# Performance work log

Hardware: AMD Instinct MI355X
Metric: run time of the kernel (lower is better)

## Reference

```python
import jax, jax.numpy as jnp
import numpy as np

B, C, R = 8, 256, 14
H_HEADS = 4
KD = 16            # key_dim
D_V = 64           # attn_ratio * key_dim
KS = 5             # dw conv kernel
N = R * R * R      # tokens


def _bias_idx():
    # replicate original offset logic: only first two coords (|dx|,|dy|) used
    pts = np.array(np.meshgrid(np.arange(R), np.arange(R), np.arange(R), indexing='ij'))
    pts = pts.reshape(3, -1).T  # (N, 3) in itertools.product order
    dx = np.abs(pts[:, 0:1] - pts[None, :, 0])  # (N, N)
    dy = np.abs(pts[:, 1:2] - pts[None, :, 1])
    return (dx * R + dy).astype(np.int32)  # (N, N), values in [0, R*R)


def setup_inputs() -> dict:
    key = jax.random.key(0)
    ks = jax.random.split(key, 12)
    cph = C // H_HEADS
    qkv_out = 2 * KD + D_V
    inp = {
        'x': jax.random.normal(ks[0], (B, C, R, R, R), jnp.float32),
        'Wqkv': jax.random.normal(ks[1], (H_HEADS, qkv_out, cph), jnp.float32) * 0.05,
        'qkv_scale': 1.0 + 0.05 * jax.random.normal(ks[2], (H_HEADS, qkv_out), jnp.float32),
        'qkv_bias': 0.05 * jax.random.normal(ks[3], (H_HEADS, qkv_out), jnp.float32),
        'Wdw': jax.random.normal(ks[4], (H_HEADS, KD, 1, KS, KS, KS), jnp.float32) * 0.05,
        'dw_scale': 1.0 + 0.05 * jax.random.normal(ks[5], (H_HEADS, KD), jnp.float32),
        'dw_bias': 0.05 * jax.random.normal(ks[6], (H_HEADS, KD), jnp.float32),
        'Wproj': jax.random.normal(ks[7], (C, D_V * H_HEADS), jnp.float32) * 0.02,
        'proj_scale': 1.0 + 0.05 * jax.random.normal(ks[8], (C,), jnp.float32),
        'proj_bias': 0.05 * jax.random.normal(ks[9], (C,), jnp.float32),
        'attention_biases': 0.02 * jax.random.normal(ks[10], (H_HEADS, R * R), jnp.float32),
        'bias_idx': jnp.asarray(_bias_idx()),
    }
    return inp


def reference(x, Wqkv, qkv_scale, qkv_bias, Wdw, dw_scale, dw_bias,
              Wproj, proj_scale, proj_bias, attention_biases, bias_idx):
    scale = KD ** (-0.5)
    ab = attention_biases[:, bias_idx]  # (h, N, N) relative-position bias gather
    feats_in = jnp.split(x, H_HEADS, axis=1)  # h x (B, C/h, R, R, R)
    dn = ('NCDHW', 'OIDHW', 'NCDHW')
    feats_out = []
    feat = feats_in[0]
    for i in range(H_HEADS):
        if i > 0:
            feat = feat + feats_in[i]
        # 1x1x1 conv QKV + fused BN (inference-style scale/shift)
        y = jnp.einsum('oc,bcxyz->boxyz', Wqkv[i], feat)
        y = y * qkv_scale[i][:, None, None, None] + qkv_bias[i][:, None, None, None]
        q = y[:, :KD]
        k = y[:, KD:2 * KD]
        v = y[:, 2 * KD:]
        # depthwise conv on q + fused BN
        q = jax.lax.conv_general_dilated(q, Wdw[i], (1, 1, 1), 'SAME',
                                         feature_group_count=KD, dimension_numbers=dn)
        q = q * dw_scale[i][:, None, None, None] + dw_bias[i][:, None, None, None]
        qf = q.reshape(B, KD, N)
        kf = k.reshape(B, KD, N)
        vf = v.reshape(B, D_V, N)
        attn = jnp.einsum('bcn,bcm->bnm', qf, kf) * scale + ab[i]  # (B, N, N)
        attn = jax.nn.softmax(attn, axis=-1)
        feat = jnp.einsum('bcm,bnm->bcn', vf, attn).reshape(B, D_V, R, R, R)
        feats_out.append(feat)
    h = jax.nn.relu(jnp.concatenate(feats_out, axis=1))  # (B, d*h, R, R, R)
    out = jnp.einsum('oc,bcxyz->boxyz', Wproj, h)
    out = out * proj_scale[:, None, None, None] + proj_bias[:, None, None, None]
    return out
```

## Files before the change

kernel.cpp:

```cpp
#include <hip/hip_runtime.h>

#define B_    8
#define C_    256
#define R_    14
#define R2    196
#define N3    2744
#define NP    2752
#define NH    4
#define KD    16
#define DV    64
#define QKVO  96
#define MT    64
#define NTILE 43
#define SPLIT 4
#define TPC   11

#define SC2   0.36067376f
#define LOG2E 1.44269504f

typedef __attribute__((ext_vector_type(8))) short short8v;
typedef __attribute__((ext_vector_type(4))) short short4v;
typedef __attribute__((ext_vector_type(4))) float float4v;

__device__ __forceinline__ int iabs(int v){ return v < 0 ? -v : v; }

__device__ __forceinline__ short f2bf(float f){
    union { float f; unsigned int u; } c; c.f = f;
    return (short)((c.u + 0x7FFFu + ((c.u >> 16) & 1u)) >> 16);
}
__device__ __forceinline__ float bf2f(short s){
    union { unsigned int u; float f; } c; c.u = ((unsigned int)(unsigned short)s) << 16;
    return c.f;
}

__global__ __launch_bounds__(256)
void wprep_kernel(const float* __restrict__ Wp, short* __restrict__ whi,
                  short* __restrict__ wlo, const float* __restrict__ Wqkv,
                  const float* __restrict__ qsc, short* __restrict__ wqhi,
                  short* __restrict__ wqlo)
{
    int i = blockIdx.x * 256 + threadIdx.x;
    {
        float w = Wp[i];
        short hi = f2bf(w);
        short lo = f2bf(w - bf2f(hi));
        whi[i] = hi; wlo[i] = lo;
    }
    if (i < NH * QKVO * 64) {
        int o_all = i >> 6;
        float w = Wqkv[i] * qsc[o_all];
        short hi = f2bf(w);
        short lo = f2bf(w - bf2f(hi));
        wqhi[i] = hi; wqlo[i] = lo;
    }
}

__global__ __launch_bounds__(256, 2)
void qkv_mfma(const float* __restrict__ x, const float* __restrict__ h,
              const short* __restrict__ wqhi, const short* __restrict__ wqlo,
              const float* __restrict__ qbi,
              float* __restrict__ q0, short* __restrict__ kbf, short* __restrict__ vbf,
              int head)
{
    __shared__ short fhi[64][72];
    __shared__ short flo[64][72];
    __shared__ float bsh[96];

    const int b = blockIdx.y;
    const int n0 = blockIdx.x * 64;
    const int t = threadIdx.x;
    const int w = t >> 6, l = t & 63, g = l >> 4, ln = l & 15;

    if (t < 96) bsh[t] = qbi[head * QKVO + t];

    {
        const int sc_ = t & 63;
        const int sng = (t >> 6) * 16;
        const float* xs = x + ((size_t)b * C_ + head * DV + sc_) * N3 + n0 + sng;
        const float* hs = h + ((size_t)b * C_ + (head - 1) * DV + sc_) * N3 + n0 + sng;
        float fv[16];
        if (n0 + sng + 15 < N3) {
#pragma unroll
            for (int e4 = 0; e4 < 4; e4++) {
                float4 xv = ((const float4*)xs)[e4];
                fv[4*e4+0] = xv.x; fv[4*e4+1] = xv.y; fv[4*e4+2] = xv.z; fv[4*e4+3] = xv.w;
            }
            if (head > 0) {
#pragma unroll
                for (int e4 = 0; e4 < 4; e4++) {
                    float4 hv = ((const float4*)hs)[e4];
                    fv[4*e4+0] += hv.x; fv[4*e4+1] += hv.y; fv[4*e4+2] += hv.z; fv[4*e4+3] += hv.w;
                }
            }
        } else {
#pragma unroll
            for (int e = 0; e < 16; e++) {
                int n = n0 + sng + e;
                float v = (n < N3) ? xs[e] : 0.f;
                if (head > 0 && n < N3) v += hs[e];
                fv[e] = v;
            }
        }
#pragma unroll
        for (int e = 0; e < 16; e++) {
            short hi = f2bf(fv[e]);
            short lo = f2bf(fv[e] - bf2f(hi));
            fhi[sng + e][sc_] = hi;
            flo[sng + e][sc_] = lo;
        }
    }
    __syncthreads();

    float4v acc[6];
#pragma unroll
    for (int os = 0; os < 6; os++) acc[os] = (float4v){0.f, 0.f, 0.f, 0.f};

    const short* wqh = wqhi + head * QKVO * 64;
    const short* wql = wqlo + head * QKVO * 64;
#pragma unroll
    for (int ck = 0; ck < 2; ck++) {
        short8v bh = *(const short8v*)&fhi[w * 16 + ln][ck * 32 + g * 8];
        short8v bl = *(const short8v*)&flo[w * 16 + ln][ck * 32 + g * 8];
#pragma unroll
        for (int os = 0; os < 6; os++) {
            size_t off = (size_t)(os * 16 + ln) * 64 + ck * 32 + g * 8;
            short8v wh = *(const short8v*)(wqh + off);
            short8v wl = *(const short8v*)(wql + off);
            acc[os] = __builtin_amdgcn_mfma_f32_16x16x32_bf16(wh, bh, acc[os], 0, 0, 0);
            acc[os] = __builtin_amdgcn_mfma_f32_16x16x32_bf16(wh, bl, acc[os], 0, 0, 0);
            acc[os] = __builtin_amdgcn_mfma_f32_16x16x32_bf16(wl, bh, acc[os], 0, 0, 0);
        }
    }

    const int n_ = n0 + w * 16 + ln;
    const bool ok = n_ < N3;
    float* qo = q0 + (size_t)b * KD * NP;
    short* ko = kbf + (size_t)b * NP * 16 + (size_t)n_ * 16;
    short* vo = vbf + (size_t)b * DV * NP;
#pragma unroll
    for (int os = 0; os < 6; os++) {
#pragma unroll
        for (int r = 0; r < 4; r++) {
            int o = os * 16 + g * 4 + r;
            float y = ok ? acc[os][r] + bsh[o] : 0.f;
            if (o < KD)            qo[(size_t)o * NP + n_] = y;
            else if (o < 2 * KD)   ko[o - KD] = f2bf(y);
            else                   vo[(size_t)(o - 2 * KD) * NP + n_] = f2bf(y);
        }
    }
}

__global__ __launch_bounds__(256)
void dwconv_kernel(float* __restrict__ q0, const float* __restrict__ Wdw,
                   const float* __restrict__ dsc, const float* __restrict__ dbi,
                   int head)
{
    __shared__ float pv[18 * 18 * 18];
    int b = blockIdx.y, c = blockIdx.x;
    int t = threadIdx.x;
    float* qc = q0 + ((size_t)b * KD + c) * NP;

    for (int i = t; i < 5832; i += 256) pv[i] = 0.f;
    __syncthreads();
    for (int i = t; i < N3; i += 256) {
        int xx = i / R2; int rem = i - xx * R2; int yy = rem / R_; int zz = rem - yy * R_;
        pv[(xx + 2) * 324 + (yy + 2) * 18 + (zz + 2)] = qc[i];
    }
    __syncthreads();

    const float* w = Wdw + (head * KD + c) * 125;
    float scl = dsc[head * KD + c], bia = dbi[head * KD + c];

    if (t < R2) {
        int x = t / R_, y = t - (t / R_) * R_;
        float acc[14];
#pragma unroll
        for (int z = 0; z < 14; z++) acc[z] = 0.f;
#pragma unroll
        for (int a = 0; a < 5; a++) {
#pragma unroll
            for (int bb = 0; bb < 5; bb++) {
                const float* base = &pv[(x + a) * 324 + (y + bb) * 18];
                float col[18];
#pragma unroll
                for (int j = 0; j < 18; j++) col[j] = base[j];
#pragma unroll
                for (int cc = 0; cc < 5; cc++) {
                    float wv = w[a * 25 + bb * 5 + cc];
#pragma unroll
                    for (int z = 0; z < 14; z++) acc[z] += wv * col[z + cc];
                }
            }
        }
        float* qo = qc + x * R2 + y * R_;
#pragma unroll
        for (int z = 0; z < 14; z++) qo[z] = acc[z] * scl + bia;
    }
}

__global__ __launch_bounds__(256, 4)
void attn_partial(const float* __restrict__ q0, const short* __restrict__ kbf,
                  const short* __restrict__ vbf, float* __restrict__ pacc,
                  float* __restrict__ pl, const float* __restrict__ abias, int head)
{
    __shared__ short ktT[64][40];
    __shared__ short vtT[64][72];
    __shared__ short plds[4][16][72];
    __shared__ int   mxa[64];
    __shared__ float ab2[200];

    const int b = blockIdx.y, z = blockIdx.z;
    const int qbase = blockIdx.x * 64;
    const int t = threadIdx.x;
    const int w = t >> 6;
    const int l = t & 63;
    const int g = l >> 4;
    const int ln = l & 15;

    if (t < 196) ab2[t] = abias[head * R2 + t] * LOG2E;
    else if (t < 200) ab2[t] = -20000.0f;

    const float* qq  = q0  + (size_t)b * KD * NP;
    const short* kbs = kbf + (size_t)b * NP * 16;
    const short* vbs = vbf + (size_t)b * DV * NP;

    {
        int mm = t & 63, dg = t >> 6;
        short4v zz = {0, 0, 0, 0};
        *(short4v*)&ktT[mm][16 + dg * 4] = zz;
    }

    const int n_my = qbase + w * 16 + ln;
    short8v qf;
#pragma unroll
    for (int j = 0; j < 8; j++) {
        int d = g * 8 + j;
        qf[j] = (d < KD) ? f2bf(qq[(size_t)d * NP + n_my]) : (short)0;
    }
    const int nmc = n_my < N3 ? n_my : 0;
    const int nx = nmc / R2, ny = (nmc - nx * R2) / R_;

    float4v acc[4];
#pragma unroll
    for (int cs = 0; cs < 4; cs++) acc[cs] = (float4v){0.f, 0.f, 0.f, 0.f};
    float lsum = 0.f;

    const int tEnd = min(z * TPC + TPC, NTILE);
    for (int t0 = z * TPC; t0 < tEnd; t0++) {
        const int m0 = t0 * MT;
        __syncthreads();
        {
            int mm = t >> 2, kq = t & 3;
            short4v kv = *(const short4v*)(kbs + (size_t)(m0 + mm) * 16 + kq * 4);
            *(short4v*)&ktT[mm][kq * 4] = kv;
        }
        {
            int c = t >> 2, mq = t & 3;
            const short* vs = vbs + (size_t)c * NP + m0 + mq * 16;
            short8v s0 = ((const short8v*)vs)[0];
            short8v s1 = ((const short8v*)vs)[1];
            *(short8v*)&vtT[c][mq * 16]     = s0;
            *(short8v*)&vtT[c][mq * 16 + 8] = s1;
        }
        if (t < 64) {
            int m = m0 + t;
            int mx, my;
            if (m < N3) { mx = m / R2; int rem = m - mx * R2; my = rem / R_; }
            else        { mx = 220; my = 220; }
            mxa[t] = (mx << 8) | my;
        }
        __syncthreads();

#pragma unroll
        for (int ms = 0; ms < 4; ms++) {
            short8v af = *(const short8v*)&ktT[ms * 16 + ln][g * 8];
            float4v zf = {0.f, 0.f, 0.f, 0.f};
            float4v s = __builtin_amdgcn_mfma_f32_16x16x32_bf16(af, qf, zf, 0, 0, 0);
            int4 pk4 = *(const int4*)&mxa[ms * 16 + g * 4];
            int pka[4] = {pk4.x, pk4.y, pk4.z, pk4.w};
            float p[4];
#pragma unroll
            for (int r = 0; r < 4; r++) {
                int mx = pka[r] >> 8, my = pka[r] & 255;
                int dx, idx;
                asm("v_sad_u32 %0, %1, %2, 0" : "=v"(dx) : "v"(nx), "v"(mx));
                int t14 = dx * 14;
                asm("v_sad_u32 %0, %1, %2, %3" : "=v"(idx) : "v"(ny), "v"(my), "v"(t14));
                idx = idx < 196 ? idx : 196;
                float lg2 = fmaf(s[r], SC2, ab2[idx]);
                p[r] = exp2f(lg2);
                lsum += p[r];
            }
            unsigned pk01, pk23;
            asm("v_cvt_pk_bf16_f32 %0, %1, %2" : "=v"(pk01) : "v"(p[0]), "v"(p[1]));
            asm("v_cvt_pk_bf16_f32 %0, %1, %2" : "=v"(pk23) : "v"(p[2]), "v"(p[3]));
            uint2 pw = make_uint2(pk01, pk23);
            *(uint2*)&plds[w][ln][ms * 16 + g * 4] = pw;
        }

#pragma unroll
        for (int ck = 0; ck < 2; ck++) {
            short8v pa = *(const short8v*)&plds[w][ln][ck * 32 + g * 8];
#pragma unroll
            for (int cs = 0; cs < 4; cs++) {
                short8v vf = *(const short8v*)&vtT[cs * 16 + ln][ck * 32 + g * 8];
                acc[cs] = __builtin_amdgcn_mfma_f32_16x16x32_bf16(pa, vf, acc[cs], 0, 0, 0);
            }
        }
    }

    lsum += __shfl_xor(lsum, 16);
    lsum += __shfl_xor(lsum, 32);

    float* pbase = pacc + (size_t)(b * SPLIT + z) * DV * NP;
    if (l < 16) {
        int n_l = qbase + w * 16 + l;
        if (n_l < N3) pl[(size_t)(b * SPLIT + z) * NP + n_l] = lsum;
    }
    const int n0w = qbase + w * 16 + g * 4;
    if (n0w < N3) {
#pragma unroll
        for (int cs = 0; cs < 4; cs++) {
            int c = cs * 16 + ln;
            *(float4v*)&pbase[(size_t)c * NP + n0w] = acc[cs];
        }
    }
}

__global__ __launch_bounds__(256)
void attn_combine(const float* __restrict__ pacc, const float* __restrict__ pl,
                  float* __restrict__ h, int head)
{
    int b = blockIdx.y;
    int ch0 = blockIdx.z * 16;
    int r = blockIdx.x * 256 + threadIdx.x;
    if (r >= N3) return;
    float l = 0.f;
#pragma unroll
    for (int z = 0; z < SPLIT; z++) l += pl[(size_t)(b * SPLIT + z) * NP + r];
    float inv = 1.f / l;
    float* hb = h + ((size_t)b * C_ + head * DV) * N3 + r;
    const float* pb = pacc + (size_t)b * SPLIT * DV * NP + r;
#pragma unroll
    for (int cc = 0; cc < 16; cc++) {
        int ch = ch0 + cc;
        float a = 0.f;
#pragma unroll
        for (int z = 0; z < SPLIT; z++) a += pb[(size_t)(z * DV + ch) * NP];
        hb[(size_t)ch * N3] = a * inv;
    }
}

__global__ __launch_bounds__(256, 2)
void proj_kernel(const float* __restrict__ h, const short* __restrict__ whi,
                 const short* __restrict__ wlo, const float* __restrict__ psc,
                 const float* __restrict__ pbi, float* __restrict__ out)
{
    __shared__ short hhi[64][40];
    __shared__ short hlo[64][40];

    const int b = blockIdx.y;
    const int n0 = blockIdx.x * 64;
    const int t = threadIdx.x;
    const int w = t >> 6, l = t & 63, g = l >> 4, ln = l & 15;

    float4v acc[4][4];
#pragma unroll
    for (int os = 0; os < 4; os++)
#pragma unroll
        for (int ns = 0; ns < 4; ns++) acc[os][ns] = (float4v){0.f, 0.f, 0.f, 0.f};

    const float* hb = h + (size_t)b * C_ * N3;
    const int sc = t >> 3;
    const int sn = (t & 7) * 8;

    for (int c0 = 0; c0 < 256; c0 += 32) {
        __syncthreads();
        {
            const float* hsrc = hb + (size_t)(c0 + sc) * N3 + n0 + sn;
            float4 f0 = ((const float4*)hsrc)[0];
            float4 f1 = ((const float4*)hsrc)[1];
            float va[8] = { f0.x, f0.y, f0.z, f0.w, f1.x, f1.y, f1.z, f1.w };
#pragma unroll
            for (int u = 0; u < 8; u++) {
                float v = va[u] > 0.f ? va[u] : 0.f;
                short hi = f2bf(v);
                short lo = f2bf(v - bf2f(hi));
                hhi[sn + u][sc] = hi;
                hlo[sn + u][sc] = lo;
            }
        }
        __syncthreads();

        short8v wh[4], wl[4];
#pragma unroll
        for (int os = 0; os < 4; os++) {
            size_t off = (size_t)(64 * w + os * 16 + ln) * 256 + c0 + g * 8;
            wh[os] = *(const short8v*)(whi + off);
            wl[os] = *(const short8v*)(wlo + off);
        }
#pragma unroll
        for (int ns = 0; ns < 4; ns++) {
            short8v bh = *(const short8v*)&hhi[ns * 16 + ln][g * 8];
            short8v bl = *(const short8v*)&hlo[ns * 16 + ln][g * 8];
#pragma unroll
            for (int os = 0; os < 4; os++) {
                acc[os][ns] = __builtin_amdgcn_mfma_f32_16x16x32_bf16(wh[os], bh, acc[os][ns], 0, 0, 0);
                acc[os][ns] = __builtin_amdgcn_mfma_f32_16x16x32_bf16(wh[os], bl, acc[os][ns], 0, 0, 0);
                acc[os][ns] = __builtin_amdgcn_mfma_f32_16x16x32_bf16(wl[os], bh, acc[os][ns], 0, 0, 0);
            }
        }
    }

    float* ob = out + (size_t)b * C_ * N3;
#pragma unroll
    for (int os = 0; os < 4; os++) {
#pragma unroll
        for (int r = 0; r < 4; r++) {
            int o = 64 * w + os * 16 + g * 4 + r;
            float s0 = psc[o], b0 = pbi[o];
#pragma unroll
            for (int ns = 0; ns < 4; ns++) {
                int n = n0 + ns * 16 + ln;
                if (n < N3) ob[(size_t)o * N3 + n] = acc[os][ns][r] * s0 + b0;
            }
        }
    }
}

extern "C" void kernel_launch(void* const* d_in, const int* in_sizes, int n_in,
                              void* d_out, int out_size, void* d_ws, size_t ws_size,
                              hipStream_t stream)
{
    const float* x    = (const float*)d_in[0];
    const float* Wqkv = (const float*)d_in[1];
    const float* qsc  = (const float*)d_in[2];
    const float* qbi  = (const float*)d_in[3];
    const float* Wdw  = (const float*)d_in[4];
    const float* dsc  = (const float*)d_in[5];
    const float* dbi  = (const float*)d_in[6];
    const float* Wp   = (const float*)d_in[7];
    const float* psc  = (const float*)d_in[8];
    const float* pbi  = (const float*)d_in[9];
    const float* ab   = (const float*)d_in[10];

    float* out = (float*)d_out;
    char*  wsb = (char*)d_ws;
    float* q0   = (float*)wsb;
    short* kbf  = (short*)(q0 + (size_t)B_ * KD * NP);
    short* vbf  = kbf + (size_t)B_ * NP * 16;
    float* h    = (float*)(vbf + (size_t)B_ * DV * NP);
    float* pacc = h + (size_t)B_ * C_ * N3;
    float* pl   = pacc + (size_t)B_ * SPLIT * DV * NP;
    short* whi  = (short*)(pl + (size_t)B_ * SPLIT * NP);
    short* wlo  = whi + 256 * 256;
    short* wqhi = wlo + 256 * 256;
    short* wqlo = wqhi + NH * QKVO * 64;

    wprep_kernel<<<256, 256, 0, stream>>>(Wp, whi, wlo, Wqkv, qsc, wqhi, wqlo);

    for (int head = 0; head < NH; head++) {
        qkv_mfma<<<dim3(43, B_), 256, 0, stream>>>(x, h, wqhi, wqlo, qbi, q0, kbf, vbf, head);
        dwconv_kernel<<<dim3(KD, B_), 256, 0, stream>>>(q0, Wdw, dsc, dbi, head);
        attn_partial<<<dim3(43, B_, SPLIT), 256, 0, stream>>>(q0, kbf, vbf, pacc, pl, ab, head);
        attn_combine<<<dim3(11, B_, 4), 256, 0, stream>>>(pacc, pl, h, head);
    }
    proj_kernel<<<dim3(43, B_), 256, 0, stream>>>(h, whi, wlo, psc, pbi, out);
}
```

Before: 338.0 us.

## Fuse split-attention combine into next head's QKV kernel, drop bias index clamp

For heads after the first, the QKV kernel now sums the four split partial accumulators, normalizes them by the summed row sums, writes the previous head's output to h, and adds it to the input feature directly. The separate combine launch and the re-read of h are removed for all but the last head. The bias table in shared memory is enlarged to 406 entries and padded columns get a sentinel coordinate of 27, so the per-element clamp on the index in the attention inner loop can be dropped. This costs more shared memory per block and puts more load traffic on the QKV kernel.

```diff
diff --git a/kernel.cpp b/kernel.cpp
--- a/kernel.cpp
+++ b/kernel.cpp
@@ -17,6 +17,7 @@
 
 #define SC2   0.36067376f
 #define LOG2E 1.44269504f
+#define ABSZ  406
 
 typedef __attribute__((ext_vector_type(8))) short short8v;
 typedef __attribute__((ext_vector_type(4))) short short4v;
@@ -56,7 +57,8 @@
 }
 
 __global__ __launch_bounds__(256, 2)
-void qkv_mfma(const float* __restrict__ x, const float* __restrict__ h,
+void qkv_mfma(const float* __restrict__ x, float* __restrict__ h,
+              const float* __restrict__ pacc, const float* __restrict__ pl,
               const short* __restrict__ wqhi, const short* __restrict__ wqlo,
               const float* __restrict__ qbi,
               float* __restrict__ q0, short* __restrict__ kbf, short* __restrict__ vbf,
@@ -65,6 +67,7 @@
     __shared__ short fhi[64][72];
     __shared__ short flo[64][72];
     __shared__ float bsh[96];
+    __shared__ float linv_s[64];
 
     const int b = blockIdx.y;
     const int n0 = blockIdx.x * 64;
@@ -73,32 +76,65 @@
 
     if (t < 96) bsh[t] = qbi[head * QKVO + t];
 
+    if (head > 0) {
+        if (t < 64) {
+            int n = n0 + t;
+            float lt = pl[(size_t)(b * SPLIT + 0) * NP + n]
+                     + pl[(size_t)(b * SPLIT + 1) * NP + n]
+                     + pl[(size_t)(b * SPLIT + 2) * NP + n]
+                     + pl[(size_t)(b * SPLIT + 3) * NP + n];
+            linv_s[t] = 1.f / lt;
+        }
+        __syncthreads();
+    }
+
     {
         const int sc_ = t & 63;
         const int sng = (t >> 6) * 16;
-        const float* xs = x + ((size_t)b * C_ + head * DV + sc_) * N3 + n0 + sng;
-        const float* hs = h + ((size_t)b * C_ + (head - 1) * DV + sc_) * N3 + n0 + sng;
+        const int nb = n0 + sng;
+        const float* xs = x + ((size_t)b * C_ + head * DV + sc_) * N3 + nb;
         float fv[16];
-        if (n0 + sng + 15 < N3) {
+        const bool fullblk = (nb + 15 < N3);
+        if (fullblk) {
 #pragma unroll
             for (int e4 = 0; e4 < 4; e4++) {
                 float4 xv = ((const float4*)xs)[e4];
                 fv[4*e4+0] = xv.x; fv[4*e4+1] = xv.y; fv[4*e4+2] = xv.z; fv[4*e4+3] = xv.w;
             }
-            if (head > 0) {
+        } else {
+#pragma unroll
+            for (int e = 0; e < 16; e++) fv[e] = (nb + e < N3) ? xs[e] : 0.f;
+        }
+        if (head > 0) {
+            const float* pb = pacc + (size_t)b * SPLIT * DV * NP + (size_t)sc_ * NP + nb;
+            float* hw = h + ((size_t)b * C_ + (head - 1) * DV + sc_) * N3 + nb;
+            const size_t zs = (size_t)DV * NP;
+            if (fullblk) {
 #pragma unroll
                 for (int e4 = 0; e4 < 4; e4++) {
-                    float4 hv = ((const float4*)hs)[e4];
-                    fv[4*e4+0] += hv.x; fv[4*e4+1] += hv.y; fv[4*e4+2] += hv.z; fv[4*e4+3] += hv.w;
+                    float4 a0 = ((const float4*)(pb         ))[e4];
+                    float4 a1 = ((const float4*)(pb +     zs))[e4];
+                    float4 a2 = ((const float4*)(pb + 2 * zs))[e4];
+                    float4 a3 = ((const float4*)(pb + 3 * zs))[e4];
+                    float hc[4];
+                    hc[0] = (a0.x + a1.x + a2.x + a3.x) * linv_s[sng + 4*e4 + 0];
+                    hc[1] = (a0.y + a1.y + a2.y + a3.y) * linv_s[sng + 4*e4 + 1];
+                    hc[2] = (a0.z + a1.z + a2.z + a3.z) * linv_s[sng + 4*e4 + 2];
+                    hc[3] = (a0.w + a1.w + a2.w + a3.w) * linv_s[sng + 4*e4 + 3];
+                    *(float4*)&hw[4*e4] = make_float4(hc[0], hc[1], hc[2], hc[3]);
+                    fv[4*e4+0] += hc[0]; fv[4*e4+1] += hc[1];
+                    fv[4*e4+2] += hc[2]; fv[4*e4+3] += hc[3];
                 }
-            }
-        } else {
-#pragma unroll
-            for (int e = 0; e < 16; e++) {
-                int n = n0 + sng + e;
-                float v = (n < N3) ? xs[e] : 0.f;
-                if (head > 0 && n < N3) v += hs[e];
-                fv[e] = v;
+            } else {
+#pragma unroll
+                for (int e = 0; e < 16; e++) {
+                    if (nb + e < N3) {
+                        float a = pb[e] + pb[e + zs] + pb[e + 2*zs] + pb[e + 3*zs];
+                        float hc = a * linv_s[sng + e];
+                        hw[e] = hc;
+                        fv[e] += hc;
+                    }
+                }
             }
         }
 #pragma unroll
@@ -207,7 +243,7 @@
     __shared__ short vtT[64][72];
     __shared__ short plds[4][16][72];
     __shared__ int   mxa[64];
-    __shared__ float ab2[200];
+    __shared__ float ab2[ABSZ];
 
     const int b = blockIdx.y, z = blockIdx.z;
     const int qbase = blockIdx.x * 64;
@@ -217,8 +253,8 @@
     const int g = l >> 4;
     const int ln = l & 15;
 
-    if (t < 196) ab2[t] = abias[head * R2 + t] * LOG2E;
-    else if (t < 200) ab2[t] = -20000.0f;
+    for (int i = t; i < ABSZ; i += 256)
+        ab2[i] = (i < 196) ? abias[head * R2 + i] * LOG2E : -20000.0f;
 
     const float* qq  = q0  + (size_t)b * KD * NP;
     const short* kbs = kbf + (size_t)b * NP * 16;
@@ -266,7 +302,7 @@
             int m = m0 + t;
             int mx, my;
             if (m < N3) { mx = m / R2; int rem = m - mx * R2; my = rem / R_; }
-            else        { mx = 220; my = 220; }
+            else        { mx = 27; my = 27; }
             mxa[t] = (mx << 8) | my;
         }
         __syncthreads();
@@ -286,7 +322,6 @@
                 asm("v_sad_u32 %0, %1, %2, 0" : "=v"(dx) : "v"(nx), "v"(mx));
                 int t14 = dx * 14;
                 asm("v_sad_u32 %0, %1, %2, %3" : "=v"(idx) : "v"(ny), "v"(my), "v"(t14));
-                idx = idx < 196 ? idx : 196;
                 float lg2 = fmaf(s[r], SC2, ab2[idx]);
                 p[r] = exp2f(lg2);
                 lsum += p[r];
@@ -460,10 +495,11 @@
     wprep_kernel<<<256, 256, 0, stream>>>(Wp, whi, wlo, Wqkv, qsc, wqhi, wqlo);
 
     for (int head = 0; head < NH; head++) {
-        qkv_mfma<<<dim3(43, B_), 256, 0, stream>>>(x, h, wqhi, wqlo, qbi, q0, kbf, vbf, head);
+        qkv_mfma<<<dim3(43, B_), 256, 0, stream>>>(x, h, pacc, pl, wqhi, wqlo, qbi,
+                                                   q0, kbf, vbf, head);
         dwconv_kernel<<<dim3(KD, B_), 256, 0, stream>>>(q0, Wdw, dsc, dbi, head);
         attn_partial<<<dim3(43, B_, SPLIT), 256, 0, stream>>>(q0, kbf, vbf, pacc, pl, ab, head);
-        attn_combine<<<dim3(11, B_, 4), 256, 0, stream>>>(pacc, pl, h, head);
-    }
+    }
+    attn_combine<<<dim3(11, B_, 4), 256, 0, stream>>>(pacc, pl, h, NH - 1);
     proj_kernel<<<dim3(43, B_), 256, 0, stream>>>(h, whi, wlo, psc, pbi, out);
 }
```

New measurement: 341.0 us. No clear change (+0.9%).
